# Performance work log

Measured on AMD Instinct MI355X. Metric: run time of the kernel, lower is better.

## Reference

```python
import jax, jax.numpy as jnp
import numpy as np

H = 64; W = 64; WS = 8; HEADS = 16; DIM = 512
HEAD_DIM = DIM // HEADS
N = WS * WS              # tokens per window
SCALE = HEAD_DIM ** -0.5
EPS = 1e-5


def _rel_pos_index():
    # Same construction as the torch buffer relative_position_index.
    coords = np.stack(np.meshgrid(np.arange(WS), np.arange(WS), indexing='ij'))  # (2, WS, WS)
    cf = coords.reshape(2, -1)                                                   # (2, N)
    rel = (cf[:, :, None] - cf[:, None, :]).transpose(1, 2, 0).copy()            # (N, N, 2)
    rel[:, :, 0] += WS - 1
    rel[:, :, 1] += WS - 1
    rel[:, :, 0] *= 2 * WS - 1
    return jnp.asarray(rel.sum(-1))  # (N, N) int

REL_IDX = _rel_pos_index()


def _layernorm(x, w, b):
    mu = jnp.mean(x, axis=-1, keepdims=True)
    var = jnp.mean(jnp.square(x - mu), axis=-1, keepdims=True)
    return (x - mu) * jax.lax.rsqrt(var + EPS) * w + b


def _window_partition(x):
    # x: (B, H, W, C) -> (nW*B, N, C)
    B, _, _, C = x.shape
    x = x.reshape(B, H // WS, WS, W // WS, WS, C).transpose(0, 1, 3, 2, 4, 5)
    return x.reshape(-1, N, C)


def _window_reverse(win, B):
    C = win.shape[-1]
    x = win.reshape(B, H // WS, W // WS, WS, WS, C).transpose(0, 1, 3, 2, 4, 5)
    return x.reshape(B, H, W, C)


def _qkv(x, w, b):
    # x: (B_, N, C); w: (C, 3C); b: (3C,) -> q,k,v each (B_, heads, N, hd)
    B_, n, C = x.shape
    t = (x @ w + b).reshape(B_, n, 3, HEADS, HEAD_DIM).transpose(2, 0, 3, 1, 4)
    return t[0], t[1], t[2]


def setup_inputs() -> dict:
    key = jax.random.key(0)
    ks = jax.random.split(key, 12)
    B = 16
    s = 0.02
    return {
        'x1': jax.random.normal(ks[0], (B, H * W, DIM), jnp.float32),
        'x2': jax.random.normal(ks[1], (B, H * W, DIM), jnp.float32),
        'norm1_w': jnp.ones((DIM,), jnp.float32),
        'norm1_b': jnp.zeros((DIM,), jnp.float32),
        'norm2_w': jnp.ones((DIM,), jnp.float32),
        'norm2_b': jnp.zeros((DIM,), jnp.float32),
        'qkv1_w': jax.random.normal(ks[2], (DIM, 3 * DIM), jnp.float32) * s,
        'qkv1_b': jnp.zeros((3 * DIM,), jnp.float32),
        'qkv2_w': jax.random.normal(ks[3], (DIM, 3 * DIM), jnp.float32) * s,
        'qkv2_b': jnp.zeros((3 * DIM,), jnp.float32),
        'rpb_table': jax.random.normal(ks[4], ((2 * WS - 1) * (2 * WS - 1), HEADS), jnp.float32) * s,
        'proj_w': jax.random.normal(ks[5], (DIM, DIM), jnp.float32) * s,
        'proj_b': jnp.zeros((DIM,), jnp.float32),
    }


def reference(x1, x2, norm1_w, norm1_b, norm2_w, norm2_b,
              qkv1_w, qkv1_b, qkv2_w, qkv2_b, rpb_table, proj_w, proj_b):
    B, L, C = x1.shape
    shortcut = x1

    # BeforeCrossAttention for each image (shift_size=0 -> no roll)
    w1 = _window_partition(_layernorm(x1, norm1_w, norm1_b).reshape(B, H, W, C))  # rescaled
    w2 = _window_partition(_layernorm(x2, norm2_w, norm2_b).reshape(B, H, W, C))  # rescaler

    q1, k1, v1 = _qkv(w1, qkv1_w, qkv1_b)   # rescaled
    q2, k2, v2 = _qkv(w2, qkv2_w, qkv2_b)   # rescaler
    # same_key_query=False: q from rescaler, k & v from rescaled
    q, k, v = q2 * SCALE, k1, v1

    attn = jnp.einsum('bhnd,bhmd->bhnm', q, k)                       # (nW*B, heads, N, N)
    bias = rpb_table[REL_IDX.reshape(-1)].reshape(N, N, HEADS).transpose(2, 0, 1)
    attn = jax.nn.softmax(attn + bias[None], axis=-1)

    out = jnp.einsum('bhnm,bhmd->bhnd', attn, v)                     # (nW*B, heads, N, hd)
    out = out.transpose(0, 2, 1, 3).reshape(-1, N, C)
    out = out @ proj_w + proj_b

    out = _window_reverse(out, B).reshape(B, L, C)
    return shortcut + out
```

## Files before the change

kernel.cpp:

```cpp
#include <hip/hip_runtime.h>
#include <hip/hip_bf16.h>

typedef __attribute__((ext_vector_type(8))) short short8;
typedef __attribute__((ext_vector_type(4))) float f32x4;

#define SCALE 0.17677669529663687f

__device__ __forceinline__ unsigned short f2bf(float f) {
    union { __hip_bfloat16 b; unsigned short u; } c;
    c.b = __float2bfloat16(f);
    return c.u;
}

__device__ __forceinline__ void gload_lds16(const unsigned short* g, unsigned short* l) {
    __builtin_amdgcn_global_load_lds((const __attribute__((address_space(1))) void*)g,
                                     (__attribute__((address_space(3))) void*)l, 16, 0, 0);
}

__global__ __launch_bounds__(256) void ln_kernel(
    const float* __restrict__ x1, const float* __restrict__ x2,
    const float* __restrict__ n1w, const float* __restrict__ n1b,
    const float* __restrict__ n2w, const float* __restrict__ n2b,
    unsigned short* __restrict__ xn1, unsigned short* __restrict__ xn2)
{
    int lane = threadIdx.x & 63;
    int row  = blockIdx.x * 4 + (threadIdx.x >> 6);
    const float* src; const float* w; const float* b; unsigned short* dst;
    if (row < 65536) {
        src = x1 + (size_t)row * 512; w = n1w; b = n1b; dst = xn1 + (size_t)row * 512;
    } else {
        size_t r = (size_t)(row - 65536);
        src = x2 + r * 512; w = n2w; b = n2b; dst = xn2 + r * 512;
    }
    float4 v0 = *(const float4*)(src + lane * 4);
    float4 v1 = *(const float4*)(src + 256 + lane * 4);
    float s = v0.x + v0.y + v0.z + v0.w + v1.x + v1.y + v1.z + v1.w;
    float q = v0.x*v0.x + v0.y*v0.y + v0.z*v0.z + v0.w*v0.w
            + v1.x*v1.x + v1.y*v1.y + v1.z*v1.z + v1.w*v1.w;
#pragma unroll
    for (int m = 1; m < 64; m <<= 1) { s += __shfl_xor(s, m); q += __shfl_xor(q, m); }
    float mu  = s * (1.0f / 512.0f);
    float var = q * (1.0f / 512.0f) - mu * mu;
    float rs  = rsqrtf(var + 1e-5f);
    float4 w0 = *(const float4*)(w + lane * 4);
    float4 w1 = *(const float4*)(w + 256 + lane * 4);
    float4 b0 = *(const float4*)(b + lane * 4);
    float4 b1 = *(const float4*)(b + 256 + lane * 4);
    ushort4 o0, o1;
    o0.x = f2bf((v0.x - mu) * rs * w0.x + b0.x);
    o0.y = f2bf((v0.y - mu) * rs * w0.y + b0.y);
    o0.z = f2bf((v0.z - mu) * rs * w0.z + b0.z);
    o0.w = f2bf((v0.w - mu) * rs * w0.w + b0.w);
    o1.x = f2bf((v1.x - mu) * rs * w1.x + b1.x);
    o1.y = f2bf((v1.y - mu) * rs * w1.y + b1.y);
    o1.z = f2bf((v1.z - mu) * rs * w1.z + b1.z);
    o1.w = f2bf((v1.w - mu) * rs * w1.w + b1.w);
    *(ushort4*)(dst + lane * 4)       = o0;
    *(ushort4*)(dst + 256 + lane * 4) = o1;
}

__global__ __launch_bounds__(256) void wconv_kernel(
    const float* __restrict__ qkv1_w, const float* __restrict__ qkv2_w,
    const float* __restrict__ proj_w,
    unsigned short* __restrict__ WqT, unsigned short* __restrict__ WkvT,
    unsigned short* __restrict__ WpT)
{
    __shared__ float tile[32][33];
    int t = blockIdx.x;
    const float* src; int ldin, c0, tn, tk; unsigned short* dst;
    if (t < 256)      { src = qkv2_w; ldin = 1536; c0 = 0;   dst = WqT;  tn = t >> 4;        tk = t & 15; }
    else if (t < 768) { int u = t - 256; src = qkv1_w; ldin = 1536; c0 = 512; dst = WkvT; tn = u >> 4; tk = u & 15; }
    else              { int u = t - 768; src = proj_w; ldin = 512;  c0 = 0;   dst = WpT;  tn = u >> 4; tk = u & 15; }
    int lx = threadIdx.x & 31, ly = threadIdx.x >> 5;
#pragma unroll
    for (int i = 0; i < 4; i++)
        tile[ly + i * 8][lx] = src[(size_t)(tk * 32 + ly + i * 8) * ldin + c0 + tn * 32 + lx];
    __syncthreads();
#pragma unroll
    for (int i = 0; i < 4; i++)
        dst[(size_t)(tn * 32 + ly + i * 8) * 512 + tk * 32 + lx] = f2bf(tile[lx][ly + i * 8]);
}


__device__ __forceinline__ void stage_unit(
    unsigned short* lds, const unsigned short* A, const unsigned short* W,
    int tile, int s, int wv, int sr, int sq, int dst_lane)
{
    int buf = (tile & 1) << 15;
    int k0  = tile * 64 + s * 32;
#pragma unroll
    for (int i = 0; i < 2; i++) {
        int R   = i * 8 + wv;
        int sub = (R * 2 + s) << 9;
        gload_lds16(A + (size_t)(R * 16 + sr) * 512 + k0 + sq * 8,
                    lds + buf + sub + dst_lane);
        gload_lds16(W + (size_t)(R * 16 + sr) * 512 + k0 + sq * 8,
                    lds + buf + 16384 + sub + dst_lane);
    }
}

template<int VM, bool DOST>
__device__ __forceinline__ void gphase(
    unsigned short* lds, const unsigned short* A, const unsigned short* W,
    f32x4 (&acc)[8][4], int tile, int s, int st_t, int st_s,
    int wr, int wc, int wv, int rdoff, int sr, int sq, int dst_lane)
{
    if constexpr (VM == 8)      asm volatile("s_waitcnt vmcnt(8)" ::: "memory");
    else if constexpr (VM == 4) asm volatile("s_waitcnt vmcnt(4)" ::: "memory");
    else                        asm volatile("s_waitcnt vmcnt(0)" ::: "memory");
    __builtin_amdgcn_s_barrier();
    __builtin_amdgcn_sched_barrier(0);
    int buf = (tile & 1) << 15;
    short8 a[8], b[4];
#pragma unroll
    for (int mi = 0; mi < 8; mi++)
        a[mi] = *(const short8*)(lds + buf + (((wr * 8 + mi) * 2 + s) << 9) + rdoff);
#pragma unroll
    for (int ni = 0; ni < 4; ni++)
        b[ni] = *(const short8*)(lds + buf + 16384 + (((wc * 4 + ni) * 2 + s) << 9) + rdoff);
    if constexpr (DOST) stage_unit(lds, A, W, st_t, st_s, wv, sr, sq, dst_lane);
    __builtin_amdgcn_s_setprio(1);
#pragma unroll
    for (int mi = 0; mi < 8; mi++)
#pragma unroll
        for (int ni = 0; ni < 4; ni++)
            acc[mi][ni] = __builtin_amdgcn_mfma_f32_16x16x32_bf16(a[mi], b[ni], acc[mi][ni], 0, 0, 0);
    __builtin_amdgcn_s_setprio(0);
}

__device__ __forceinline__ void gemm256(
    unsigned short* lds, const unsigned short* A, const unsigned short* W,
    f32x4 (&acc)[8][4])
{
    int tid = threadIdx.x, lane = tid & 63, wv = tid >> 6;
    int wr = wv >> 2, wc = wv & 3;
    int lr = lane & 15, lk = lane >> 4;
    int rdoff    = lr * 32 + ((lk ^ ((lr >> 1) & 3)) << 3);
    int sr       = lane >> 2;
    int sq       = (lane & 3) ^ ((sr >> 1) & 3);
    int dst_lane = lane * 8;

    stage_unit(lds, A, W, 0, 0, wv, sr, sq, dst_lane);
    stage_unit(lds, A, W, 0, 1, wv, sr, sq, dst_lane);
    stage_unit(lds, A, W, 1, 0, wv, sr, sq, dst_lane);
    stage_unit(lds, A, W, 1, 1, wv, sr, sq, dst_lane);

    gphase<8,false>(lds, A, W, acc, 0, 0, 0, 0, wr, wc, wv, rdoff, sr, sq, dst_lane);
    gphase<8,true >(lds, A, W, acc, 0, 1, 2, 0, wr, wc, wv, rdoff, sr, sq, dst_lane);
    gphase<8,true >(lds, A, W, acc, 1, 0, 2, 1, wr, wc, wv, rdoff, sr, sq, dst_lane);
    gphase<8,true >(lds, A, W, acc, 1, 1, 3, 0, wr, wc, wv, rdoff, sr, sq, dst_lane);
    gphase<8,true >(lds, A, W, acc, 2, 0, 3, 1, wr, wc, wv, rdoff, sr, sq, dst_lane);
    gphase<8,true >(lds, A, W, acc, 2, 1, 4, 0, wr, wc, wv, rdoff, sr, sq, dst_lane);
    gphase<8,true >(lds, A, W, acc, 3, 0, 4, 1, wr, wc, wv, rdoff, sr, sq, dst_lane);
    gphase<8,true >(lds, A, W, acc, 3, 1, 5, 0, wr, wc, wv, rdoff, sr, sq, dst_lane);
    gphase<8,true >(lds, A, W, acc, 4, 0, 5, 1, wr, wc, wv, rdoff, sr, sq, dst_lane);
    gphase<8,true >(lds, A, W, acc, 4, 1, 6, 0, wr, wc, wv, rdoff, sr, sq, dst_lane);
    gphase<8,true >(lds, A, W, acc, 5, 0, 6, 1, wr, wc, wv, rdoff, sr, sq, dst_lane);
    gphase<8,true >(lds, A, W, acc, 5, 1, 7, 0, wr, wc, wv, rdoff, sr, sq, dst_lane);
    gphase<8,true >(lds, A, W, acc, 6, 0, 7, 1, wr, wc, wv, rdoff, sr, sq, dst_lane);
    gphase<8,false>(lds, A, W, acc, 6, 1, 0, 0, wr, wc, wv, rdoff, sr, sq, dst_lane);
    gphase<4,false>(lds, A, W, acc, 7, 0, 0, 0, wr, wc, wv, rdoff, sr, sq, dst_lane);
    gphase<0,false>(lds, A, W, acc, 7, 1, 0, 0, wr, wc, wv, rdoff, sr, sq, dst_lane);
}

__global__ __launch_bounds__(512) void qkv_gemm256(
    const unsigned short* __restrict__ XN1, const unsigned short* __restrict__ XN2,
    const unsigned short* __restrict__ WqT, const unsigned short* __restrict__ WkvT,
    const float* __restrict__ qkv1_b, const float* __restrict__ qkv2_b,
    unsigned short* __restrict__ Qb, unsigned short* __restrict__ KVb)
{
    __shared__ unsigned short lds[65536];
    int bid = blockIdx.x;
    int wg  = (bid & 7) * 192 + (bid >> 3);
    int mb  = wg / 6, nb = wg % 6;
    f32x4 acc[8][4];
#pragma unroll
    for (int mi = 0; mi < 8; mi++)
#pragma unroll
        for (int ni = 0; ni < 4; ni++) { f32x4 z = {0.f,0.f,0.f,0.f}; acc[mi][ni] = z; }
    const unsigned short* A; const unsigned short* W;
    if (nb < 2) { A = XN2 + (size_t)mb * 256 * 512; W = WqT  + (size_t)nb * 256 * 512; }
    else        { A = XN1 + (size_t)mb * 256 * 512; W = WkvT + (size_t)(nb - 2) * 256 * 512; }
    gemm256(lds, A, W, acc);

    int lane = threadIdx.x & 63, wv = threadIdx.x >> 6;
    int wr = wv >> 2, wc = wv & 3, lr = lane & 15, lk = lane >> 4;
    int base_m = mb * 256 + wr * 128;
    if (nb < 2) {
#pragma unroll
        for (int ni = 0; ni < 4; ni++) {
            int col = nb * 256 + wc * 64 + ni * 16 + lr;
            float bias = qkv2_b[col];
#pragma unroll
            for (int mi = 0; mi < 8; mi++)
#pragma unroll
                for (int ii = 0; ii < 4; ii++) {
                    int row = base_m + mi * 16 + lk * 4 + ii;
                    Qb[(size_t)row * 512 + col] = f2bf((acc[mi][ni][ii] + bias) * SCALE);
                }
        }
    } else {
#pragma unroll
        for (int ni = 0; ni < 4; ni++) {
            int col = (nb - 2) * 256 + wc * 64 + ni * 16 + lr;
            float bias = qkv1_b[512 + col];
#pragma unroll
            for (int mi = 0; mi < 8; mi++)
#pragma unroll
                for (int ii = 0; ii < 4; ii++) {
                    int row = base_m + mi * 16 + lk * 4 + ii;
                    KVb[(size_t)row * 1024 + col] = f2bf(acc[mi][ni][ii] + bias);
                }
        }
    }
}

__global__ __launch_bounds__(512) void proj_gemm256(
    const unsigned short* __restrict__ AO, const unsigned short* __restrict__ WpT,
    const float* __restrict__ proj_b, const float* __restrict__ x1,
    float* __restrict__ out)
{
    __shared__ unsigned short lds[65536];
    int bid = blockIdx.x;
    int wg  = (bid & 7) * 64 + (bid >> 3);
    int mb  = wg >> 1, nb = wg & 1;
    f32x4 acc[8][4];
#pragma unroll
    for (int mi = 0; mi < 8; mi++)
#pragma unroll
        for (int ni = 0; ni < 4; ni++) { f32x4 z = {0.f,0.f,0.f,0.f}; acc[mi][ni] = z; }
    gemm256(lds, AO + (size_t)mb * 256 * 512, WpT + (size_t)nb * 256 * 512, acc);

    int lane = threadIdx.x & 63, wv = threadIdx.x >> 6;
    int wr = wv >> 2, wc = wv & 3, lr = lane & 15, lk = lane >> 4;
    int base_m = mb * 256 + wr * 128;
#pragma unroll
    for (int ni = 0; ni < 4; ni++) {
        int col = nb * 256 + wc * 64 + ni * 16 + lr;
        float bias = proj_b[col];
#pragma unroll
        for (int mi = 0; mi < 8; mi++)
#pragma unroll
            for (int ii = 0; ii < 4; ii++) {
                int row = base_m + mi * 16 + lk * 4 + ii;
                out[(size_t)row * 512 + col] = acc[mi][ni][ii] + bias + x1[(size_t)row * 512 + col];
            }
    }
}

__global__ __launch_bounds__(256) void attn_kernel(
    const unsigned short* __restrict__ Qb, const unsigned short* __restrict__ KVb,
    const float* __restrict__ rpb, unsigned short* __restrict__ AO)
{
    __shared__ unsigned short sV[4][64 * 32];
    __shared__ unsigned short sP[4][64 * 64];
    int wv = threadIdx.x >> 6, lane = threadIdx.x & 63;
    int lr = lane & 15, lk = lane >> 4;
    int u = blockIdx.x * 4 + wv;
    int win = u >> 4, h = u & 15;
    int b = win >> 6, wi = win & 63;
    int rowbase = b * 4096 + (wi >> 3) * 512 + (wi & 7) * 8;
    unsigned short* myV = sV[wv];
    unsigned short* myP = sP[wv];

#pragma unroll
    for (int i = 0; i < 4; i++) {
        int c = i * 64 + lane;
        int t = c >> 2, cc = c & 3;
        int grow = rowbase + (t >> 3) * 64 + (t & 7);
        *(short8*)(myV + t * 32 + cc * 8) =
            *(const short8*)(KVb + (size_t)grow * 1024 + 512 + h * 32 + cc * 8);
    }
    short8 qf[4], kf[4];
#pragma unroll
    for (int fr = 0; fr < 4; fr++) {
        int t = 16 * fr + lr;
        int grow = rowbase + (t >> 3) * 64 + (t & 7);
        qf[fr] = *(const short8*)(Qb  + (size_t)grow * 512  + h * 32 + lk * 8);
        kf[fr] = *(const short8*)(KVb + (size_t)grow * 1024 + h * 32 + lk * 8);
    }
    f32x4 s[4][4];
#pragma unroll
    for (int fr = 0; fr < 4; fr++)
#pragma unroll
        for (int fc = 0; fc < 4; fc++) { f32x4 z = {0.f,0.f,0.f,0.f}; s[fr][fc] = z; }
#pragma unroll
    for (int fr = 0; fr < 4; fr++)
#pragma unroll
        for (int fc = 0; fc < 4; fc++)
            s[fr][fc] = __builtin_amdgcn_mfma_f32_16x16x32_bf16(qf[fr], kf[fc], s[fr][fc], 0, 0, 0);

    float rinv[4][4];
#pragma unroll
    for (int fr = 0; fr < 4; fr++) {
#pragma unroll
        for (int i = 0; i < 4; i++) {
            int n = 16 * fr + 4 * lk + i;
#pragma unroll
            for (int fc = 0; fc < 4; fc++) {
                int m = 16 * fc + lr;
                int idx = ((n >> 3) - (m >> 3) + 7) * 15 + (n & 7) - (m & 7) + 7;
                s[fr][fc][i] += rpb[idx * 16 + h];
            }
            float v = fmaxf(fmaxf(s[fr][0][i], s[fr][1][i]), fmaxf(s[fr][2][i], s[fr][3][i]));
            v = fmaxf(v, __shfl_xor(v, 1)); v = fmaxf(v, __shfl_xor(v, 2));
            v = fmaxf(v, __shfl_xor(v, 4)); v = fmaxf(v, __shfl_xor(v, 8));
            float sum = 0.f;
#pragma unroll
            for (int fc = 0; fc < 4; fc++) {
                float e = __expf(s[fr][fc][i] - v);
                s[fr][fc][i] = e; sum += e;
            }
            sum += __shfl_xor(sum, 1); sum += __shfl_xor(sum, 2);
            sum += __shfl_xor(sum, 4); sum += __shfl_xor(sum, 8);
            rinv[fr][i] = 1.0f / sum;
#pragma unroll
            for (int fc = 0; fc < 4; fc++) {
                int m = 16 * fc + lr;
                int chunk = (m >> 3) ^ (n & 7);
                myP[n * 64 + chunk * 8 + (m & 7)] = f2bf(s[fr][fc][i]);
            }
        }
    }
    __syncthreads();

    f32x4 o[4][2];
#pragma unroll
    for (int fr = 0; fr < 4; fr++)
#pragma unroll
        for (int nj = 0; nj < 2; nj++) { f32x4 z = {0.f,0.f,0.f,0.f}; o[fr][nj] = z; }
#pragma unroll
    for (int mk = 0; mk < 2; mk++) {
        short8 pa[4];
#pragma unroll
        for (int fr = 0; fr < 4; fr++) {
            int n = 16 * fr + lr;
            int chunk = (4 * mk + lk) ^ (n & 7);
            pa[fr] = *(const short8*)(myP + n * 64 + chunk * 8);
        }
#pragma unroll
        for (int nj = 0; nj < 2; nj++) {
            short8 vb;
#pragma unroll
            for (int j = 0; j < 8; j++)
                vb[j] = (short)myV[(32 * mk + 8 * lk + j) * 32 + 16 * nj + lr];
#pragma unroll
            for (int fr = 0; fr < 4; fr++)
                o[fr][nj] = __builtin_amdgcn_mfma_f32_16x16x32_bf16(pa[fr], vb, o[fr][nj], 0, 0, 0);
        }
    }
#pragma unroll
    for (int fr = 0; fr < 4; fr++)
#pragma unroll
        for (int nj = 0; nj < 2; nj++)
#pragma unroll
            for (int i = 0; i < 4; i++) {
                int t = 16 * fr + 4 * lk + i;
                int grow = rowbase + (t >> 3) * 64 + (t & 7);
                AO[(size_t)grow * 512 + h * 32 + 16 * nj + lr] = f2bf(o[fr][nj][i] * rinv[fr][i]);
            }
}

extern "C" void kernel_launch(void* const* d_in, const int* in_sizes, int n_in,
                              void* d_out, int out_size, void* d_ws, size_t ws_size,
                              hipStream_t stream)
{
    const float* x1     = (const float*)d_in[0];
    const float* x2     = (const float*)d_in[1];
    const float* n1w    = (const float*)d_in[2];
    const float* n1b    = (const float*)d_in[3];
    const float* n2w    = (const float*)d_in[4];
    const float* n2b    = (const float*)d_in[5];
    const float* qkv1_w = (const float*)d_in[6];
    const float* qkv1_b = (const float*)d_in[7];
    const float* qkv2_w = (const float*)d_in[8];
    const float* qkv2_b = (const float*)d_in[9];
    const float* rpb    = (const float*)d_in[10];
    const float* proj_w = (const float*)d_in[11];
    const float* proj_b = (const float*)d_in[12];
    float* out = (float*)d_out;

    char* ws = (char*)d_ws;
    const size_t SZ = 67108864;
    unsigned short* XN1  = (unsigned short*)(ws);
    unsigned short* XN2  = (unsigned short*)(ws + SZ);
    unsigned short* Qb   = (unsigned short*)(ws + 2 * SZ);
    unsigned short* KVb  = (unsigned short*)(ws + 3 * SZ);
    unsigned short* WqT  = (unsigned short*)(ws + 5 * SZ);
    unsigned short* WkvT = WqT + 512 * 512;
    unsigned short* WpT  = WkvT + 1024 * 512;
    unsigned short* AO   = XN2;

    hipLaunchKernelGGL(ln_kernel,     dim3(32768), dim3(256), 0, stream,
                       x1, x2, n1w, n1b, n2w, n2b, XN1, XN2);
    hipLaunchKernelGGL(wconv_kernel,  dim3(1024),  dim3(256), 0, stream,
                       qkv1_w, qkv2_w, proj_w, WqT, WkvT, WpT);
    hipLaunchKernelGGL(qkv_gemm256,   dim3(1536),  dim3(512), 0, stream,
                       XN1, XN2, WqT, WkvT, qkv1_b, qkv2_b, Qb, KVb);
    hipLaunchKernelGGL(attn_kernel,   dim3(4096),  dim3(256), 0, stream,
                       Qb, KVb, rpb, AO);
    hipLaunchKernelGGL(proj_gemm256,  dim3(512),   dim3(512), 0, stream,
                       AO, WpT, proj_b, x1, out);
}
```

Before: 675.9 us.

## Restructure GEMM pipeline to per-tile phases and precompute relative position bias

New measurement: 665.9 us. No clear change (-1.5%).

```diff
diff --git a/kernel.cpp b/kernel.cpp
--- a/kernel.cpp
+++ b/kernel.cpp
@@ -99,33 +99,51 @@
     }
 }
 
-template<int VM, bool DOST>
-__device__ __forceinline__ void gphase(
+template<bool LAST, bool DOST>
+__device__ __forceinline__ void gtile(
     unsigned short* lds, const unsigned short* A, const unsigned short* W,
-    f32x4 (&acc)[8][4], int tile, int s, int st_t, int st_s,
+    f32x4 (&acc)[8][4], int tile, int st_t,
     int wr, int wc, int wv, int rdoff, int sr, int sq, int dst_lane)
 {
-    if constexpr (VM == 8)      asm volatile("s_waitcnt vmcnt(8)" ::: "memory");
-    else if constexpr (VM == 4) asm volatile("s_waitcnt vmcnt(4)" ::: "memory");
-    else                        asm volatile("s_waitcnt vmcnt(0)" ::: "memory");
+    if constexpr (LAST) asm volatile("s_waitcnt vmcnt(0)" ::: "memory");
+    else                asm volatile("s_waitcnt vmcnt(8)" ::: "memory");
     __builtin_amdgcn_s_barrier();
     __builtin_amdgcn_sched_barrier(0);
     int buf = (tile & 1) << 15;
-    short8 a[8], b[4];
-#pragma unroll
-    for (int mi = 0; mi < 8; mi++)
-        a[mi] = *(const short8*)(lds + buf + (((wr * 8 + mi) * 2 + s) << 9) + rdoff);
+    short8 a0[8], b0[4], a1[8], b1[4];
+#pragma unroll
+    for (int mi = 0; mi < 8; mi++)
+        a0[mi] = *(const short8*)(lds + buf + (((wr * 8 + mi) * 2 + 0) << 9) + rdoff);
 #pragma unroll
     for (int ni = 0; ni < 4; ni++)
-        b[ni] = *(const short8*)(lds + buf + 16384 + (((wc * 4 + ni) * 2 + s) << 9) + rdoff);
-    if constexpr (DOST) stage_unit(lds, A, W, st_t, st_s, wv, sr, sq, dst_lane);
+        b0[ni] = *(const short8*)(lds + buf + 16384 + (((wc * 4 + ni) * 2 + 0) << 9) + rdoff);
     __builtin_amdgcn_s_setprio(1);
 #pragma unroll
     for (int mi = 0; mi < 8; mi++)
 #pragma unroll
         for (int ni = 0; ni < 4; ni++)
-            acc[mi][ni] = __builtin_amdgcn_mfma_f32_16x16x32_bf16(a[mi], b[ni], acc[mi][ni], 0, 0, 0);
+            acc[mi][ni] = __builtin_amdgcn_mfma_f32_16x16x32_bf16(a0[mi], b0[ni], acc[mi][ni], 0, 0, 0);
     __builtin_amdgcn_s_setprio(0);
+#pragma unroll
+    for (int mi = 0; mi < 8; mi++)
+        a1[mi] = *(const short8*)(lds + buf + (((wr * 8 + mi) * 2 + 1) << 9) + rdoff);
+#pragma unroll
+    for (int ni = 0; ni < 4; ni++)
+        b1[ni] = *(const short8*)(lds + buf + 16384 + (((wc * 4 + ni) * 2 + 1) << 9) + rdoff);
+    __builtin_amdgcn_s_setprio(1);
+#pragma unroll
+    for (int mi = 0; mi < 8; mi++)
+#pragma unroll
+        for (int ni = 0; ni < 4; ni++)
+            acc[mi][ni] = __builtin_amdgcn_mfma_f32_16x16x32_bf16(a1[mi], b1[ni], acc[mi][ni], 0, 0, 0);
+    __builtin_amdgcn_s_setprio(0);
+    __builtin_amdgcn_sched_barrier(0);
+    __builtin_amdgcn_s_barrier();
+    __builtin_amdgcn_sched_barrier(0);
+    if constexpr (DOST) {
+        stage_unit(lds, A, W, st_t, 0, wv, sr, sq, dst_lane);
+        stage_unit(lds, A, W, st_t, 1, wv, sr, sq, dst_lane);
+    }
 }
 
 __device__ __forceinline__ void gemm256(
@@ -145,22 +163,14 @@
     stage_unit(lds, A, W, 1, 0, wv, sr, sq, dst_lane);
     stage_unit(lds, A, W, 1, 1, wv, sr, sq, dst_lane);
 
-    gphase<8,false>(lds, A, W, acc, 0, 0, 0, 0, wr, wc, wv, rdoff, sr, sq, dst_lane);
-    gphase<8,true >(lds, A, W, acc, 0, 1, 2, 0, wr, wc, wv, rdoff, sr, sq, dst_lane);
-    gphase<8,true >(lds, A, W, acc, 1, 0, 2, 1, wr, wc, wv, rdoff, sr, sq, dst_lane);
-    gphase<8,true >(lds, A, W, acc, 1, 1, 3, 0, wr, wc, wv, rdoff, sr, sq, dst_lane);
-    gphase<8,true >(lds, A, W, acc, 2, 0, 3, 1, wr, wc, wv, rdoff, sr, sq, dst_lane);
-    gphase<8,true >(lds, A, W, acc, 2, 1, 4, 0, wr, wc, wv, rdoff, sr, sq, dst_lane);
-    gphase<8,true >(lds, A, W, acc, 3, 0, 4, 1, wr, wc, wv, rdoff, sr, sq, dst_lane);
-    gphase<8,true >(lds, A, W, acc, 3, 1, 5, 0, wr, wc, wv, rdoff, sr, sq, dst_lane);
-    gphase<8,true >(lds, A, W, acc, 4, 0, 5, 1, wr, wc, wv, rdoff, sr, sq, dst_lane);
-    gphase<8,true >(lds, A, W, acc, 4, 1, 6, 0, wr, wc, wv, rdoff, sr, sq, dst_lane);
-    gphase<8,true >(lds, A, W, acc, 5, 0, 6, 1, wr, wc, wv, rdoff, sr, sq, dst_lane);
-    gphase<8,true >(lds, A, W, acc, 5, 1, 7, 0, wr, wc, wv, rdoff, sr, sq, dst_lane);
-    gphase<8,true >(lds, A, W, acc, 6, 0, 7, 1, wr, wc, wv, rdoff, sr, sq, dst_lane);
-    gphase<8,false>(lds, A, W, acc, 6, 1, 0, 0, wr, wc, wv, rdoff, sr, sq, dst_lane);
-    gphase<4,false>(lds, A, W, acc, 7, 0, 0, 0, wr, wc, wv, rdoff, sr, sq, dst_lane);
-    gphase<0,false>(lds, A, W, acc, 7, 1, 0, 0, wr, wc, wv, rdoff, sr, sq, dst_lane);
+    gtile<false, true >(lds, A, W, acc, 0, 2, wr, wc, wv, rdoff, sr, sq, dst_lane);
+    gtile<false, true >(lds, A, W, acc, 1, 3, wr, wc, wv, rdoff, sr, sq, dst_lane);
+    gtile<false, true >(lds, A, W, acc, 2, 4, wr, wc, wv, rdoff, sr, sq, dst_lane);
+    gtile<false, true >(lds, A, W, acc, 3, 5, wr, wc, wv, rdoff, sr, sq, dst_lane);
+    gtile<false, true >(lds, A, W, acc, 4, 6, wr, wc, wv, rdoff, sr, sq, dst_lane);
+    gtile<false, true >(lds, A, W, acc, 5, 7, wr, wc, wv, rdoff, sr, sq, dst_lane);
+    gtile<false, false>(lds, A, W, acc, 6, 0, wr, wc, wv, rdoff, sr, sq, dst_lane);
+    gtile<true , false>(lds, A, W, acc, 7, 0, wr, wc, wv, rdoff, sr, sq, dst_lane);
 }
 
 __global__ __launch_bounds__(512) void qkv_gemm256(
@@ -248,9 +258,30 @@
     }
 }
 
+__global__ __launch_bounds__(256) void bias_pre(
+    const float* __restrict__ rpb, float* __restrict__ biasC)
+{
+    int h = blockIdx.x;
+    int lane = threadIdx.x & 63;
+    int fr = threadIdx.x >> 6;
+    int lk = lane >> 4, lr = lane & 15;
+#pragma unroll
+    for (int fc = 0; fc < 4; fc++) {
+        float4 v;
+#pragma unroll
+        for (int i = 0; i < 4; i++) {
+            int n = 16 * fr + 4 * lk + i;
+            int m = 16 * fc + lr;
+            int idx = ((n >> 3) - (m >> 3) + 7) * 15 + (n & 7) - (m & 7) + 7;
+            (&v.x)[i] = rpb[idx * 16 + h];
+        }
+        *(float4*)(biasC + (((h * 4 + fr) * 4 + fc) << 8) + (lane << 2)) = v;
+    }
+}
+
 __global__ __launch_bounds__(256) void attn_kernel(
     const unsigned short* __restrict__ Qb, const unsigned short* __restrict__ KVb,
-    const float* __restrict__ rpb, unsigned short* __restrict__ AO)
+    const float* __restrict__ biasC, unsigned short* __restrict__ AO)
 {
     __shared__ unsigned short sV[4][64 * 32];
     __shared__ unsigned short sP[4][64 * 64];
@@ -290,18 +321,20 @@
         for (int fc = 0; fc < 4; fc++)
             s[fr][fc] = __builtin_amdgcn_mfma_f32_16x16x32_bf16(qf[fr], kf[fc], s[fr][fc], 0, 0, 0);
 
+    const float* bch = biasC + (h << 12);
     float rinv[4][4];
 #pragma unroll
     for (int fr = 0; fr < 4; fr++) {
+        f32x4 bb[4];
+#pragma unroll
+        for (int fc = 0; fc < 4; fc++)
+            bb[fc] = *(const f32x4*)(bch + (((fr << 2) + fc) << 8) + (lane << 2));
 #pragma unroll
         for (int i = 0; i < 4; i++) {
             int n = 16 * fr + 4 * lk + i;
 #pragma unroll
-            for (int fc = 0; fc < 4; fc++) {
-                int m = 16 * fc + lr;
-                int idx = ((n >> 3) - (m >> 3) + 7) * 15 + (n & 7) - (m & 7) + 7;
-                s[fr][fc][i] += rpb[idx * 16 + h];
-            }
+            for (int fc = 0; fc < 4; fc++)
+                s[fr][fc][i] += bb[fc][i];
             float v = fmaxf(fmaxf(s[fr][0][i], s[fr][1][i]), fmaxf(s[fr][2][i], s[fr][3][i]));
             v = fmaxf(v, __shfl_xor(v, 1)); v = fmaxf(v, __shfl_xor(v, 2));
             v = fmaxf(v, __shfl_xor(v, 4)); v = fmaxf(v, __shfl_xor(v, 8));
@@ -390,6 +423,7 @@
     unsigned short* WkvT = WqT + 512 * 512;
     unsigned short* WpT  = WkvT + 1024 * 512;
     unsigned short* AO   = XN2;
+    float* biasC = (float*)ws;
 
     hipLaunchKernelGGL(ln_kernel,     dim3(32768), dim3(256), 0, stream,
                        x1, x2, n1w, n1b, n2w, n2b, XN1, XN2);
@@ -397,8 +431,10 @@
                        qkv1_w, qkv2_w, proj_w, WqT, WkvT, WpT);
     hipLaunchKernelGGL(qkv_gemm256,   dim3(1536),  dim3(512), 0, stream,
                        XN1, XN2, WqT, WkvT, qkv1_b, qkv2_b, Qb, KVb);
+    hipLaunchKernelGGL(bias_pre,      dim3(16),    dim3(256), 0, stream,
+                       rpb, biasC);
     hipLaunchKernelGGL(attn_kernel,   dim3(4096),  dim3(256), 0, stream,
-                       Qb, KVb, rpb, AO);
+                       Qb, KVb, biasC, AO);
     hipLaunchKernelGGL(proj_gemm256,  dim3(512),   dim3(512), 0, stream,
                        AO, WpT, proj_b, x1, out);
 }
```
